# Optimization experiments

Measured on AMD Instinct MI355X. Metric: run time of the kernel, lower is better.

Reference implementation:

```python
import jax, jax.numpy as jnp
import numpy as np

B, C_IN, C_QKV, N = 8, 12, 36, 4096

def setup_inputs() -> dict:
    key = jax.random.key(0)
    ks = jax.random.split(key, 9)
    s_in = 1.0 / np.sqrt(C_IN)
    s_o = 1.0 / np.sqrt(C_QKV)
    return {
        "x": jax.random.normal(ks[0], (B, C_IN, N), dtype=jnp.float32),
        "wq": jax.random.uniform(ks[1], (C_QKV, C_IN), jnp.float32, -s_in, s_in),
        "bq": jax.random.uniform(ks[2], (C_QKV,), jnp.float32, -s_in, s_in),
        "wk": jax.random.uniform(ks[3], (C_QKV, C_IN), jnp.float32, -s_in, s_in),
        "bk": jax.random.uniform(ks[4], (C_QKV,), jnp.float32, -s_in, s_in),
        "wv": jax.random.uniform(ks[5], (C_QKV, C_IN), jnp.float32, -s_in, s_in),
        "bv": jax.random.uniform(ks[6], (C_QKV,), jnp.float32, -s_in, s_in),
        "wo": jax.random.uniform(ks[7], (C_IN, C_QKV), jnp.float32, -s_o, s_o),
        "bo": jax.random.uniform(ks[8], (C_IN,), jnp.float32, -s_o, s_o),
    }

def _conv1x1(w, b, x):
    # 1x1 Conv1d == channel-mixing matmul: [o,i] @ [b,i,n] -> [b,o,n]
    return jnp.einsum('oi,bin->bon', w, x) + b[None, :, None]

def reference(x, wq, bq, wk, bk, wv, bv, wo, bo):
    scale = 1.0 / jnp.sqrt(jnp.float32(x.shape[1]))  # 1/sqrt(12)
    q = _conv1x1(wq, bq, x)  # [B, 36, N]
    k = _conv1x1(wk, bk, x)
    v = _conv1x1(wv, bv, x)
    # inter = k^T @ q : scores[b,n,m] = sum_c k[b,c,n] * q[b,c,m]
    scores = jnp.einsum('bcn,bcm->bnm', k, q) * scale  # [B, N, N]
    weights = jax.nn.softmax(scores, axis=-1)
    attn = jnp.einsum('bcn,bnm->bcm', v, weights)  # v @ weights, [B, 36, N]
    return _conv1x1(wo, bo, attn)  # [B, 12, N]
```

## Files before the change

kernel.cpp:

```cpp
#include <hip/hip_runtime.h>
#include <hip/hip_bf16.h>
#include <math.h>

#define B 8
#define CIN 12
#define CQ 36
#define CP 48
#define N 4096
#define SCALE 0.28867513459481287f
#define LOG2E 1.4426950408889634f
#define ZSPLIT 8
#define NCHUNK (N / ZSPLIT)
#define NT (NCHUNK / 32)
#define MSPLIT 2

typedef __attribute__((ext_vector_type(4)))  short bf4_t;
typedef __attribute__((ext_vector_type(8)))  short bf8_t;
typedef __attribute__((ext_vector_type(16))) float f32x16;
typedef __attribute__((ext_vector_type(4)))  float f32x4;

__device__ __forceinline__ unsigned short f2bf(float x) {
  unsigned int u = __float_as_uint(x);
  u += 0x7FFFu + ((u >> 16) & 1u);
  return (unsigned short)(u >> 16);
}

#if __has_builtin(__builtin_amdgcn_cvt_pk_bf16_f32)
typedef __attribute__((ext_vector_type(2))) __bf16 bf16x2_t;
__device__ __forceinline__ unsigned pk2bf(float a, float b) {
  bf16x2_t v = __builtin_amdgcn_cvt_pk_bf16_f32(a, b);
  return __builtin_bit_cast(unsigned, v);
}
#else
__device__ __forceinline__ unsigned pk2bf(float a, float b) {
  return (__float_as_uint(a) >> 16) | (__float_as_uint(b) & 0xFFFF0000u);
}
#endif

__device__ __forceinline__ float bf2f(unsigned short u) {
  return __uint_as_float((unsigned)u << 16);
}

__device__ __forceinline__ float exp2fast(float x) {
#if __has_builtin(__builtin_amdgcn_exp2f)
  return __builtin_amdgcn_exp2f(x);
#else
  return exp2f(x);
#endif
}

__device__ __forceinline__ f32x4 mfma16(bf4_t a, bf4_t b, f32x4 c) {
#if __has_builtin(__builtin_amdgcn_mfma_f32_16x16x16bf16_1k)
  return __builtin_amdgcn_mfma_f32_16x16x16bf16_1k(a, b, c, 0, 0, 0);
#else
  bf8_t a8 = {a[0], a[1], a[2], a[3], 0, 0, 0, 0};
  bf8_t b8 = {b[0], b[1], b[2], b[3], 0, 0, 0, 0};
  return __builtin_amdgcn_mfma_f32_16x16x32_bf16(a8, b8, c, 0, 0, 0);
#endif
}

__device__ __forceinline__ bf8_t lds_bf8(const unsigned short* p) {
  uint2 a = *(const uint2*)p;
  uint2 b = *(const uint2*)(p + 4);
  uint4 r{a.x, a.y, b.x, b.y};
  return __builtin_bit_cast(bf8_t, r);
}
__device__ __forceinline__ void wlds16(unsigned short* p, uint4 v) {
  *(uint2*)p = uint2{v.x, v.y};
  *(uint2*)(p + 4) = uint2{v.z, v.w};
}

__global__ __launch_bounds__(256) void qkv_kernel(
    const float* __restrict__ x,
    const float* __restrict__ wq, const float* __restrict__ bq,
    const float* __restrict__ wk, const float* __restrict__ bk,
    const float* __restrict__ wv, const float* __restrict__ bv,
    unsigned short* __restrict__ qT, unsigned short* __restrict__ kT,
    unsigned short* __restrict__ vbf) {
  __shared__ float sw[CQ * CIN];
  __shared__ float sb[CQ];
  int z = blockIdx.y;
  const float* w  = (z == 0) ? wq : (z == 1) ? wk : wv;
  const float* bb = (z == 0) ? bq : (z == 1) ? bk : bv;
  float scale = (z == 1) ? SCALE * LOG2E : 1.0f;
  int tid = threadIdx.x;
  for (int e = tid; e < CQ * CIN; e += 256) sw[e] = w[e] * scale;
  if (tid < CQ) sb[tid] = bb[tid] * scale;
  __syncthreads();
  int gid = blockIdx.x * 256 + tid;
  int b = gid >> 12;
  int n = gid & (N - 1);
  float xv[CIN];
#pragma unroll
  for (int i = 0; i < CIN; ++i) xv[i] = x[(b * CIN + i) * N + n];
  if (z == 2) {
#pragma unroll
    for (int o = 0; o < CQ; ++o) {
      float a = sb[o];
#pragma unroll
      for (int i = 0; i < CIN; ++i) a += sw[o * CIN + i] * xv[i];
      vbf[((size_t)b * CP + o) * N + n] = f2bf(a);
    }
  } else {
    __attribute__((aligned(16))) unsigned row[CP / 2];
#pragma unroll
    for (int o = 0; o < CQ; o += 2) {
      float a0 = sb[o], a1 = sb[o + 1];
#pragma unroll
      for (int i = 0; i < CIN; ++i) {
        float xi = xv[i];
        a0 += sw[o * CIN + i] * xi;
        a1 += sw[(o + 1) * CIN + i] * xi;
      }
      row[o / 2] = (unsigned)f2bf(a0) | ((unsigned)f2bf(a1) << 16);
    }
    row[18] = (z == 0) ? 0x3F803F80u : 0u;
#pragma unroll
    for (int o = 19; o < CP / 2; ++o) row[o] = 0;
    unsigned short* dst = ((z == 0) ? qT : kT) + ((size_t)b * N + n) * CP;
#pragma unroll
    for (int i = 0; i < 6; ++i) *(uint4*)(dst + 8 * i) = *(const uint4*)&row[4 * i];
  }
}

__global__ __launch_bounds__(256) void stats_kernel(
    const unsigned short* __restrict__ qT, const unsigned short* __restrict__ kT,
    float* __restrict__ psum) {
  __shared__ float red[4][64];
  int tid = threadIdx.x, lane = tid & 63, wave = tid >> 6;
  int b = blockIdx.y, nblk = blockIdx.x, ms = blockIdx.z;
  int l31 = lane & 31, h = lane >> 5;
  int n0 = nblk * 64;
  size_t bN = (size_t)b * N;
  const unsigned short* krow0 = kT + (bN + n0 + l31) * CP + h * 8;
  const unsigned short* krow1 = krow0 + (size_t)32 * CP;
  bf8_t a0 = *(const bf8_t*)(krow0);
  bf8_t a1 = *(const bf8_t*)(krow0 + 16);
  bf8_t a2 = *(const bf8_t*)(krow0 + 32);
  bf8_t a3 = *(const bf8_t*)(krow1);
  bf8_t a4 = *(const bf8_t*)(krow1 + 16);
  bf8_t a5 = *(const bf8_t*)(krow1 + 32);
  float rs0[16], rs1[16];
#pragma unroll
  for (int r = 0; r < 16; ++r) { rs0[r] = 0.f; rs1[r] = 0.f; }
  const int MW = N / MSPLIT / 4;
  const unsigned short* qbase =
      qT + (bN + ms * (N / MSPLIT) + wave * MW + l31) * CP + h * 8;
#pragma unroll 2
  for (int t = 0; t < MW / 32; ++t) {
    const unsigned short* qrow2 = qbase + (size_t)t * 32 * CP;
    bf8_t b0 = *(const bf8_t*)(qrow2);
    bf8_t b1 = *(const bf8_t*)(qrow2 + 16);
    bf8_t b2 = *(const bf8_t*)(qrow2 + 32);
    f32x16 S0, S1;
#pragma unroll
    for (int r = 0; r < 16; ++r) { S0[r] = 0.f; S1[r] = 0.f; }
    S0 = __builtin_amdgcn_mfma_f32_32x32x16_bf16(a0, b0, S0, 0, 0, 0);
    S0 = __builtin_amdgcn_mfma_f32_32x32x16_bf16(a1, b1, S0, 0, 0, 0);
    S0 = __builtin_amdgcn_mfma_f32_32x32x16_bf16(a2, b2, S0, 0, 0, 0);
    S1 = __builtin_amdgcn_mfma_f32_32x32x16_bf16(a3, b0, S1, 0, 0, 0);
    S1 = __builtin_amdgcn_mfma_f32_32x32x16_bf16(a4, b1, S1, 0, 0, 0);
    S1 = __builtin_amdgcn_mfma_f32_32x32x16_bf16(a5, b2, S1, 0, 0, 0);
#pragma unroll
    for (int r = 0; r < 16; ++r) {
      rs0[r] += exp2fast(S0[r]);
      rs1[r] += exp2fast(S1[r]);
    }
  }
#pragma unroll
  for (int off = 16; off >= 1; off >>= 1)
#pragma unroll
    for (int r = 0; r < 16; ++r) {
      rs0[r] += __shfl_xor(rs0[r], off, 32);
      rs1[r] += __shfl_xor(rs1[r], off, 32);
    }
  if (l31 == 0) {
#pragma unroll
    for (int r = 0; r < 16; ++r) {
      int row = (r & 3) + 8 * (r >> 2) + 4 * h;
      red[wave][row] = rs0[r];
      red[wave][32 + row] = rs1[r];
    }
  }
  __syncthreads();
  if (tid < 64) {
    float s = red[0][tid] + red[1][tid] + red[2][tid] + red[3][tid];
    psum[((size_t)ms * B + b) * N + n0 + tid] = s;
  }
}

__global__ __launch_bounds__(256) void prep_kernel(
    const float* __restrict__ psum, unsigned short* __restrict__ kT,
    float* __restrict__ out, const float* __restrict__ bo) {
  int bx = blockIdx.x, tid = threadIdx.x;
  if (bx < B * N / 256) {
    int gid = bx * 256 + tid;
    float L = 0.f;
#pragma unroll
    for (int ms = 0; ms < MSPLIT; ++ms) L += psum[(size_t)ms * B * N + gid];
    float t = -__log2f(L);
    unsigned short hi = f2bf(t);
    unsigned short lo = f2bf(t - bf2f(hi));
    size_t base = (size_t)gid * CP;
    kT[base + 36] = hi;
    kT[base + 37] = lo;
  } else {
    int gid = (bx - B * N / 256) * 256 + tid;
    int e4 = gid * 4;
    int i = (e4 >> 12) % CIN;
    float bv = bo[i];
    *(float4*)(out + e4) = float4{bv, bv, bv, bv};
  }
}

__global__ __launch_bounds__(256, 3) void attn_kernel(
    const unsigned short* __restrict__ qT, const unsigned short* __restrict__ kT,
    const unsigned short* __restrict__ vbf, const float* __restrict__ wo,
    float* __restrict__ out) {
  __shared__ unsigned short kbuf[2][32 * 52];
  __shared__ unsigned short vbuf[2][48 * 36];
  __shared__ unsigned short plds[4][2][32 * 40];
  int tid = threadIdx.x, lane = tid & 63, wave = tid >> 6;
  int b = blockIdx.y, z = blockIdx.z, mblk = blockIdx.x;
  int l31 = lane & 31, h = lane >> 5, l15 = lane & 15, q4 = lane >> 4;
  int m0 = mblk * 256 + wave * 64;
  size_t bN = (size_t)b * N;
  bool isK0 = tid < 192;
  int r0row = isK0 ? (tid / 6) : ((tid - 192) >> 2);
  int r0c   = isK0 ? (tid % 6) : ((tid - 192) & 3);
  const unsigned short* s0 = isK0
      ? kT + (bN + z * NCHUNK + r0row) * CP + r0c * 8
      : vbf + ((size_t)b * CP + r0row) * N + z * NCHUNK + r0c * 8;
  int s0stride = isK0 ? 32 * CP : 32;
  unsigned short* dst0 = isK0 ? &kbuf[0][r0row * 52 + r0c * 8]
                              : &vbuf[0][r0row * 36 + r0c * 8];
  int dbs0 = isK0 ? 32 * 52 : 48 * 36;
  bool has1 = tid < 128;
  int r1row = (tid >> 2) + 16;
  int r1c = tid & 3;
  const unsigned short* s1 =
      vbf + ((size_t)b * CP + r1row) * N + z * NCHUNK + r1c * 8;
  unsigned short* dst1 = &vbuf[0][r1row * 36 + r1c * 8];
  const int dbs1 = 48 * 36;
  bf8_t qb[2][3];
#pragma unroll
  for (int mt = 0; mt < 2; ++mt) {
    const unsigned short* qrow = qT + (bN + m0 + mt * 32 + l31) * CP + h * 8;
    qb[mt][0] = *(const bf8_t*)(qrow);
    qb[mt][1] = *(const bf8_t*)(qrow + 16);
    qb[mt][2] = *(const bf8_t*)(qrow + 32);
  }
  bf4_t woa[3];
#pragma unroll
  for (int ct = 0; ct < 3; ++ct) {
    float4 w4 = {0.f, 0.f, 0.f, 0.f};
    int col = 16 * ct + q4 * 4;
    if (l15 < CIN && col < CQ) w4 = *(const float4*)(wo + l15 * CQ + col);
    woa[ct] = bf4_t{(short)f2bf(w4.x), (short)f2bf(w4.y),
                    (short)f2bf(w4.z), (short)f2bf(w4.w)};
  }
  f32x4 acc[2][3][2];
#pragma unroll
  for (int mt = 0; mt < 2; ++mt)
#pragma unroll
    for (int ct = 0; ct < 3; ++ct)
#pragma unroll
      for (int hm = 0; hm < 2; ++hm)
#pragma unroll
        for (int r = 0; r < 4; ++r) acc[mt][ct][hm][r] = 0.f;
  uint4 r0 = *(const uint4*)s0; s0 += s0stride;
  uint4 r1{0, 0, 0, 0};
  if (has1) { r1 = *(const uint4*)s1; s1 += 32; }
  wlds16(dst0, r0);
  if (has1) wlds16(dst1, r1);
  __syncthreads();
  for (int t = 0; t < NT; ++t) {
    int buf = t & 1;
    if (t + 1 < NT) {
      r0 = *(const uint4*)s0; s0 += s0stride;
      if (has1) { r1 = *(const uint4*)s1; s1 += 32; }
    }
    const unsigned short* kb = kbuf[buf];
    const unsigned short* vb = vbuf[buf];
    bf8_t a0 = lds_bf8(kb + l31 * 52 + h * 8);
    bf8_t a1 = lds_bf8(kb + l31 * 52 + h * 8 + 16);
    bf8_t a2 = lds_bf8(kb + l31 * 52 + h * 8 + 32);
#pragma unroll
    for (int mt = 0; mt < 2; ++mt) {
      f32x16 S;
#pragma unroll
      for (int r = 0; r < 16; ++r) S[r] = 0.f;
      S = __builtin_amdgcn_mfma_f32_32x32x16_bf16(a0, qb[mt][0], S, 0, 0, 0);
      S = __builtin_amdgcn_mfma_f32_32x32x16_bf16(a1, qb[mt][1], S, 0, 0, 0);
      S = __builtin_amdgcn_mfma_f32_32x32x16_bf16(a2, qb[mt][2], S, 0, 0, 0);
      unsigned short* pl = plds[wave][mt];
#pragma unroll
      for (int qd = 0; qd < 4; ++qd) {
        uint2 pk;
        pk.x = pk2bf(exp2fast(S[4 * qd + 0]), exp2fast(S[4 * qd + 1]));
        pk.y = pk2bf(exp2fast(S[4 * qd + 2]), exp2fast(S[4 * qd + 3]));
        *(uint2*)&pl[l31 * 40 + 8 * qd + 4 * h] = pk;
      }
    }
    bf8_t v0 = lds_bf8(vb + (0 * 16 + l15) * 36 + q4 * 8);
    bf8_t v1 = lds_bf8(vb + (1 * 16 + l15) * 36 + q4 * 8);
    bf8_t v2 = lds_bf8(vb + (2 * 16 + l15) * 36 + q4 * 8);
#pragma unroll
    for (int mt = 0; mt < 2; ++mt) {
      const unsigned short* pl = plds[wave][mt];
      bf8_t pb0 = *(const bf8_t*)&pl[l15 * 40 + q4 * 8];
      bf8_t pb1 = *(const bf8_t*)&pl[(16 + l15) * 40 + q4 * 8];
      acc[mt][0][0] = __builtin_amdgcn_mfma_f32_16x16x32_bf16(v0, pb0, acc[mt][0][0], 0, 0, 0);
      acc[mt][0][1] = __builtin_amdgcn_mfma_f32_16x16x32_bf16(v0, pb1, acc[mt][0][1], 0, 0, 0);
      acc[mt][1][0] = __builtin_amdgcn_mfma_f32_16x16x32_bf16(v1, pb0, acc[mt][1][0], 0, 0, 0);
      acc[mt][1][1] = __builtin_amdgcn_mfma_f32_16x16x32_bf16(v1, pb1, acc[mt][1][1], 0, 0, 0);
      acc[mt][2][0] = __builtin_amdgcn_mfma_f32_16x16x32_bf16(v2, pb0, acc[mt][2][0], 0, 0, 0);
      acc[mt][2][1] = __builtin_amdgcn_mfma_f32_16x16x32_bf16(v2, pb1, acc[mt][2][1], 0, 0, 0);
    }
    if (t + 1 < NT) {
      int nb = buf ^ 1;
      wlds16(dst0 + nb * dbs0, r0);
      if (has1) wlds16(dst1 + nb * dbs1, r1);
    }
    __syncthreads();
  }
#pragma unroll
  for (int mt = 0; mt < 2; ++mt)
#pragma unroll
    for (int hm = 0; hm < 2; ++hm) {
      f32x4 po = {0.f, 0.f, 0.f, 0.f};
#pragma unroll
      for (int ct = 0; ct < 3; ++ct) {
        union { uint2 u; bf4_t v; } pb;
        pb.u.x = pk2bf(acc[mt][ct][hm][0], acc[mt][ct][hm][1]);
        pb.u.y = pk2bf(acc[mt][ct][hm][2], acc[mt][ct][hm][3]);
        po = mfma16(woa[ct], pb.v, po);
      }
      if (q4 < 3) {
        float* ob = out + ((size_t)b * CIN + q4 * 4) * N + m0 + mt * 32 + hm * 16 + l15;
#pragma unroll
        for (int r = 0; r < 4; ++r) atomicAdd(ob + (size_t)r * N, po[r]);
      }
    }
}

extern "C" void kernel_launch(void* const* d_in, const int* in_sizes, int n_in,
                              void* d_out, int out_size, void* d_ws, size_t ws_size,
                              hipStream_t stream) {
  const float* x  = (const float*)d_in[0];
  const float* wq = (const float*)d_in[1];
  const float* bq = (const float*)d_in[2];
  const float* wk = (const float*)d_in[3];
  const float* bk = (const float*)d_in[4];
  const float* wv = (const float*)d_in[5];
  const float* bv = (const float*)d_in[6];
  const float* wo = (const float*)d_in[7];
  const float* bo = (const float*)d_in[8];
  float* out = (float*)d_out;

  char* ws = (char*)d_ws;
  unsigned short* qT  = (unsigned short*)ws;
  unsigned short* kT  = (unsigned short*)(ws + 3145728);
  unsigned short* vbf = (unsigned short*)(ws + 2 * 3145728);
  float* psum = (float*)(ws + 3 * 3145728);

  qkv_kernel<<<dim3(B * N / 256, 3), 256, 0, stream>>>(x, wq, bq, wk, bk, wv, bv,
                                                       qT, kT, vbf);
  stats_kernel<<<dim3(N / 64, B, MSPLIT), 256, 0, stream>>>(qT, kT, psum);
  prep_kernel<<<B * N / 256 + B * CIN * N / 1024, 256, 0, stream>>>(psum, kT, out, bo);
  attn_kernel<<<dim3(N / 256, B, ZSPLIT), 256, 0, stream>>>(qT, kT, vbf, wo, out);
}
```

Measured before the change: 137.7 us.

## Fuse four attention kernels into one persistent cooperative kernel with grid syncs

Adds a cooperative persistent kernel that runs the QKV projection, output bias init, softmax row-sum statistics and attention+output projection as phases separated by grid-wide syncs, replacing four separate launches. The log-sum computation formerly in a prep kernel is folded into the attention tile loader. This targets launch overhead and inter-kernel gaps, at the cost of grid barrier latency, a capped grid size that forces blocks to loop over work units, and LDS reuse through a union. The original multi-kernel path remains as a fallback when cooperative launch is unsupported.

```diff
diff --git a/kernel.cpp b/kernel.cpp
--- a/kernel.cpp
+++ b/kernel.cpp
@@ -1,6 +1,9 @@
 #include <hip/hip_runtime.h>
 #include <hip/hip_bf16.h>
+#include <hip/hip_cooperative_groups.h>
 #include <math.h>
+
+namespace cg = cooperative_groups;
 
 #define B 8
 #define CIN 12
@@ -68,6 +71,294 @@
 __device__ __forceinline__ void wlds16(unsigned short* p, uint4 v) {
   *(uint2*)p = uint2{v.x, v.y};
   *(uint2*)(p + 4) = uint2{v.z, v.w};
+}
+
+struct SmemAttn {
+  unsigned short kbuf[2][32 * 52];
+  unsigned short vbuf[2][48 * 36];
+  unsigned short plds[4][2][32 * 40];
+};
+union Smem {
+  SmemAttn at;
+  struct { float sw[CQ * CIN]; float sb[CQ]; } qk;
+  float red[4][64];
+};
+
+__global__ __launch_bounds__(256, 2) void fused_kernel(
+    const float* __restrict__ x,
+    const float* __restrict__ wq, const float* __restrict__ bq,
+    const float* __restrict__ wk, const float* __restrict__ bk,
+    const float* __restrict__ wv, const float* __restrict__ bv,
+    const float* __restrict__ wo, const float* __restrict__ bo,
+    unsigned short* __restrict__ qT, unsigned short* __restrict__ kT,
+    unsigned short* __restrict__ vbf, float* __restrict__ psum,
+    float* __restrict__ out) {
+  __shared__ Smem sm;
+  int tid = threadIdx.x;
+  int G = gridDim.x;
+  int lane = tid & 63, wave = tid >> 6;
+  int l31 = lane & 31, h = lane >> 5, l15 = lane & 15, q4 = lane >> 4;
+
+  for (int u = blockIdx.x; u < 384 + 384; u += G) {
+    if (u < 384) {
+      int z = u >> 7;
+      int nblk = u & 127;
+      const float* w  = (z == 0) ? wq : (z == 1) ? wk : wv;
+      const float* bb = (z == 0) ? bq : (z == 1) ? bk : bv;
+      float scale = (z == 1) ? SCALE * LOG2E : 1.0f;
+      __syncthreads();
+      for (int e = tid; e < CQ * CIN; e += 256) sm.qk.sw[e] = w[e] * scale;
+      if (tid < CQ) sm.qk.sb[tid] = bb[tid] * scale;
+      __syncthreads();
+      int gid = nblk * 256 + tid;
+      int b = gid >> 12;
+      int n = gid & (N - 1);
+      float xv[CIN];
+#pragma unroll
+      for (int i = 0; i < CIN; ++i) xv[i] = x[(b * CIN + i) * N + n];
+      if (z == 2) {
+#pragma unroll
+        for (int o = 0; o < CQ; ++o) {
+          float a = sm.qk.sb[o];
+#pragma unroll
+          for (int i = 0; i < CIN; ++i) a += sm.qk.sw[o * CIN + i] * xv[i];
+          vbf[((size_t)b * CP + o) * N + n] = f2bf(a);
+        }
+      } else {
+        __attribute__((aligned(16))) unsigned row[CP / 2];
+#pragma unroll
+        for (int o = 0; o < CQ; o += 2) {
+          float a0 = sm.qk.sb[o], a1 = sm.qk.sb[o + 1];
+#pragma unroll
+          for (int i = 0; i < CIN; ++i) {
+            float xi = xv[i];
+            a0 += sm.qk.sw[o * CIN + i] * xi;
+            a1 += sm.qk.sw[(o + 1) * CIN + i] * xi;
+          }
+          row[o / 2] = (unsigned)f2bf(a0) | ((unsigned)f2bf(a1) << 16);
+        }
+        row[18] = (z == 0) ? 0x3F803F80u : 0u;
+#pragma unroll
+        for (int o = 19; o < CP / 2; ++o) row[o] = 0;
+        unsigned short* dst = ((z == 0) ? qT : kT) + ((size_t)b * N + n) * CP;
+#pragma unroll
+        for (int i = 0; i < 6; ++i) *(uint4*)(dst + 8 * i) = *(const uint4*)&row[4 * i];
+      }
+    } else {
+      int gid4 = (u - 384) * 256 + tid;
+      int e4 = gid4 * 4;
+      int i = (e4 >> 12) % CIN;
+      float bvv = bo[i];
+      *(float4*)(out + e4) = float4{bvv, bvv, bvv, bvv};
+    }
+  }
+  __threadfence();
+  cg::this_grid().sync();
+
+  for (int u = blockIdx.x; u < 64 * B * MSPLIT; u += G) {
+    int nblk = u & 63, b = (u >> 6) & 7, ms = u >> 9;
+    __syncthreads();
+    int n0 = nblk * 64;
+    size_t bN = (size_t)b * N;
+    const unsigned short* krow0 = kT + (bN + n0 + l31) * CP + h * 8;
+    const unsigned short* krow1 = krow0 + (size_t)32 * CP;
+    bf8_t a0 = *(const bf8_t*)(krow0);
+    bf8_t a1 = *(const bf8_t*)(krow0 + 16);
+    bf8_t a2 = *(const bf8_t*)(krow0 + 32);
+    bf8_t a3 = *(const bf8_t*)(krow1);
+    bf8_t a4 = *(const bf8_t*)(krow1 + 16);
+    bf8_t a5 = *(const bf8_t*)(krow1 + 32);
+    float rs0[16], rs1[16];
+#pragma unroll
+    for (int r = 0; r < 16; ++r) { rs0[r] = 0.f; rs1[r] = 0.f; }
+    const int MW = N / MSPLIT / 4;
+    const unsigned short* qbase =
+        qT + (bN + ms * (N / MSPLIT) + wave * MW + l31) * CP + h * 8;
+#pragma unroll 2
+    for (int t = 0; t < MW / 32; ++t) {
+      const unsigned short* qrow2 = qbase + (size_t)t * 32 * CP;
+      bf8_t b0 = *(const bf8_t*)(qrow2);
+      bf8_t b1 = *(const bf8_t*)(qrow2 + 16);
+      bf8_t b2 = *(const bf8_t*)(qrow2 + 32);
+      f32x16 S0, S1;
+#pragma unroll
+      for (int r = 0; r < 16; ++r) { S0[r] = 0.f; S1[r] = 0.f; }
+      S0 = __builtin_amdgcn_mfma_f32_32x32x16_bf16(a0, b0, S0, 0, 0, 0);
+      S0 = __builtin_amdgcn_mfma_f32_32x32x16_bf16(a1, b1, S0, 0, 0, 0);
+      S0 = __builtin_amdgcn_mfma_f32_32x32x16_bf16(a2, b2, S0, 0, 0, 0);
+      S1 = __builtin_amdgcn_mfma_f32_32x32x16_bf16(a3, b0, S1, 0, 0, 0);
+      S1 = __builtin_amdgcn_mfma_f32_32x32x16_bf16(a4, b1, S1, 0, 0, 0);
+      S1 = __builtin_amdgcn_mfma_f32_32x32x16_bf16(a5, b2, S1, 0, 0, 0);
+#pragma unroll
+      for (int r = 0; r < 16; ++r) {
+        rs0[r] += exp2fast(S0[r]);
+        rs1[r] += exp2fast(S1[r]);
+      }
+    }
+#pragma unroll
+    for (int off = 16; off >= 1; off >>= 1)
+#pragma unroll
+      for (int r = 0; r < 16; ++r) {
+        rs0[r] += __shfl_xor(rs0[r], off, 32);
+        rs1[r] += __shfl_xor(rs1[r], off, 32);
+      }
+    if (l31 == 0) {
+#pragma unroll
+      for (int r = 0; r < 16; ++r) {
+        int row = (r & 3) + 8 * (r >> 2) + 4 * h;
+        sm.red[wave][row] = rs0[r];
+        sm.red[wave][32 + row] = rs1[r];
+      }
+    }
+    __syncthreads();
+    if (tid < 64) {
+      float s = sm.red[0][tid] + sm.red[1][tid] + sm.red[2][tid] + sm.red[3][tid];
+      psum[((size_t)ms * B + b) * N + n0 + tid] = s;
+    }
+  }
+  __threadfence();
+  cg::this_grid().sync();
+
+  bf4_t woa[3];
+#pragma unroll
+  for (int ct = 0; ct < 3; ++ct) {
+    float4 w4 = {0.f, 0.f, 0.f, 0.f};
+    int col = 16 * ct + q4 * 4;
+    if (l15 < CIN && col < CQ) w4 = *(const float4*)(wo + l15 * CQ + col);
+    woa[ct] = bf4_t{(short)f2bf(w4.x), (short)f2bf(w4.y),
+                    (short)f2bf(w4.z), (short)f2bf(w4.w)};
+  }
+  for (int u = blockIdx.x; u < 16 * B * ZSPLIT; u += G) {
+    int mblk = u & 15, b = (u >> 4) & 7, z = u >> 7;
+    __syncthreads();
+    int m0 = mblk * 256 + wave * 64;
+    size_t bN = (size_t)b * N;
+    bool isK0 = tid < 192;
+    int r0row = isK0 ? (tid / 6) : ((tid - 192) >> 2);
+    int r0c   = isK0 ? (tid % 6) : ((tid - 192) & 3);
+    const unsigned short* s0 = isK0
+        ? kT + (bN + z * NCHUNK + r0row) * CP + r0c * 8
+        : vbf + ((size_t)b * CP + r0row) * N + z * NCHUNK + r0c * 8;
+    int s0stride = isK0 ? 32 * CP : 32;
+    unsigned short* dst0 = isK0 ? &sm.at.kbuf[0][r0row * 52 + r0c * 8]
+                                : &sm.at.vbuf[0][r0row * 36 + r0c * 8];
+    int dbs0 = isK0 ? 32 * 52 : 48 * 36;
+    bool has1 = tid < 128;
+    int r1row = (tid >> 2) + 16;
+    int r1c = tid & 3;
+    const unsigned short* s1 =
+        vbf + ((size_t)b * CP + r1row) * N + z * NCHUNK + r1c * 8;
+    unsigned short* dst1 = &sm.at.vbuf[0][r1row * 36 + r1c * 8];
+    const int dbs1 = 48 * 36;
+    bool isP = isK0 && (r0c == 4);
+    const float* pL = psum + bN + z * NCHUNK + r0row;
+    bf8_t qb[2][3];
+#pragma unroll
+    for (int mt = 0; mt < 2; ++mt) {
+      const unsigned short* qrow = qT + (bN + m0 + mt * 32 + l31) * CP + h * 8;
+      qb[mt][0] = *(const bf8_t*)(qrow);
+      qb[mt][1] = *(const bf8_t*)(qrow + 16);
+      qb[mt][2] = *(const bf8_t*)(qrow + 32);
+    }
+    f32x4 acc[2][3][2];
+#pragma unroll
+    for (int mt = 0; mt < 2; ++mt)
+#pragma unroll
+      for (int ct = 0; ct < 3; ++ct)
+#pragma unroll
+        for (int hm = 0; hm < 2; ++hm)
+#pragma unroll
+          for (int r = 0; r < 4; ++r) acc[mt][ct][hm][r] = 0.f;
+    uint4 r0 = *(const uint4*)s0; s0 += s0stride;
+    uint4 r1{0, 0, 0, 0};
+    if (has1) { r1 = *(const uint4*)s1; s1 += 32; }
+    float Lp = 0.f;
+    if (isP) { Lp = pL[0] + pL[(size_t)B * N]; pL += 32; }
+    if (isP) {
+      float tl = -__log2f(Lp);
+      unsigned short hi = f2bf(tl);
+      unsigned short lo = f2bf(tl - bf2f(hi));
+      r0.z = (unsigned)hi | ((unsigned)lo << 16);
+    }
+    wlds16(dst0, r0);
+    if (has1) wlds16(dst1, r1);
+    __syncthreads();
+    for (int t = 0; t < NT; ++t) {
+      int buf = t & 1;
+      if (t + 1 < NT) {
+        r0 = *(const uint4*)s0; s0 += s0stride;
+        if (has1) { r1 = *(const uint4*)s1; s1 += 32; }
+        if (isP) { Lp = pL[0] + pL[(size_t)B * N]; pL += 32; }
+      }
+      const unsigned short* kb = sm.at.kbuf[buf];
+      const unsigned short* vb = sm.at.vbuf[buf];
+      bf8_t a0 = lds_bf8(kb + l31 * 52 + h * 8);
+      bf8_t a1 = lds_bf8(kb + l31 * 52 + h * 8 + 16);
+      bf8_t a2 = lds_bf8(kb + l31 * 52 + h * 8 + 32);
+#pragma unroll
+      for (int mt = 0; mt < 2; ++mt) {
+        f32x16 S;
+#pragma unroll
+        for (int r = 0; r < 16; ++r) S[r] = 0.f;
+        S = __builtin_amdgcn_mfma_f32_32x32x16_bf16(a0, qb[mt][0], S, 0, 0, 0);
+        S = __builtin_amdgcn_mfma_f32_32x32x16_bf16(a1, qb[mt][1], S, 0, 0, 0);
+        S = __builtin_amdgcn_mfma_f32_32x32x16_bf16(a2, qb[mt][2], S, 0, 0, 0);
+        unsigned short* pl = sm.at.plds[wave][mt];
+#pragma unroll
+        for (int qd = 0; qd < 4; ++qd) {
+          uint2 pk;
+          pk.x = pk2bf(exp2fast(S[4 * qd + 0]), exp2fast(S[4 * qd + 1]));
+          pk.y = pk2bf(exp2fast(S[4 * qd + 2]), exp2fast(S[4 * qd + 3]));
+          *(uint2*)&pl[l31 * 40 + 8 * qd + 4 * h] = pk;
+        }
+      }
+      bf8_t v0 = lds_bf8(vb + (0 * 16 + l15) * 36 + q4 * 8);
+      bf8_t v1 = lds_bf8(vb + (1 * 16 + l15) * 36 + q4 * 8);
+      bf8_t v2 = lds_bf8(vb + (2 * 16 + l15) * 36 + q4 * 8);
+#pragma unroll
+      for (int mt = 0; mt < 2; ++mt) {
+        const unsigned short* pl = sm.at.plds[wave][mt];
+        bf8_t pb0 = *(const bf8_t*)&pl[l15 * 40 + q4 * 8];
+        bf8_t pb1 = *(const bf8_t*)&pl[(16 + l15) * 40 + q4 * 8];
+        acc[mt][0][0] = __builtin_amdgcn_mfma_f32_16x16x32_bf16(v0, pb0, acc[mt][0][0], 0, 0, 0);
+        acc[mt][0][1] = __builtin_amdgcn_mfma_f32_16x16x32_bf16(v0, pb1, acc[mt][0][1], 0, 0, 0);
+        acc[mt][1][0] = __builtin_amdgcn_mfma_f32_16x16x32_bf16(v1, pb0, acc[mt][1][0], 0, 0, 0);
+        acc[mt][1][1] = __builtin_amdgcn_mfma_f32_16x16x32_bf16(v1, pb1, acc[mt][1][1], 0, 0, 0);
+        acc[mt][2][0] = __builtin_amdgcn_mfma_f32_16x16x32_bf16(v2, pb0, acc[mt][2][0], 0, 0, 0);
+        acc[mt][2][1] = __builtin_amdgcn_mfma_f32_16x16x32_bf16(v2, pb1, acc[mt][2][1], 0, 0, 0);
+      }
+      if (t + 1 < NT) {
+        int nb = buf ^ 1;
+        if (isP) {
+          float tl = -__log2f(Lp);
+          unsigned short hi = f2bf(tl);
+          unsigned short lo = f2bf(tl - bf2f(hi));
+          r0.z = (unsigned)hi | ((unsigned)lo << 16);
+        }
+        wlds16(dst0 + nb * dbs0, r0);
+        if (has1) wlds16(dst1 + nb * dbs1, r1);
+      }
+      __syncthreads();
+    }
+#pragma unroll
+    for (int mt = 0; mt < 2; ++mt)
+#pragma unroll
+      for (int hm = 0; hm < 2; ++hm) {
+        f32x4 po = {0.f, 0.f, 0.f, 0.f};
+#pragma unroll
+        for (int ct = 0; ct < 3; ++ct) {
+          union { uint2 u; bf4_t v; } pb;
+          pb.u.x = pk2bf(acc[mt][ct][hm][0], acc[mt][ct][hm][1]);
+          pb.u.y = pk2bf(acc[mt][ct][hm][2], acc[mt][ct][hm][3]);
+          po = mfma16(woa[ct], pb.v, po);
+        }
+        if (q4 < 3) {
+          float* ob = out + ((size_t)b * CIN + q4 * 4) * N + m0 + mt * 32 + hm * 16 + l15;
+#pragma unroll
+          for (int r = 0; r < 4; ++r) atomicAdd(ob + (size_t)r * N, po[r]);
+        }
+      }
+  }
 }
 
 __global__ __launch_bounds__(256) void qkv_kernel(
@@ -364,9 +655,33 @@
   unsigned short* vbf = (unsigned short*)(ws + 2 * 3145728);
   float* psum = (float*)(ws + 3 * 3145728);
 
-  qkv_kernel<<<dim3(B * N / 256, 3), 256, 0, stream>>>(x, wq, bq, wk, bk, wv, bv,
-                                                       qT, kT, vbf);
-  stats_kernel<<<dim3(N / 64, B, MSPLIT), 256, 0, stream>>>(qT, kT, psum);
-  prep_kernel<<<B * N / 256 + B * CIN * N / 1024, 256, 0, stream>>>(psum, kT, out, bo);
-  attn_kernel<<<dim3(N / 256, B, ZSPLIT), 256, 0, stream>>>(qT, kT, vbf, wo, out);
-}
+  static int coop = -1;
+  static int grid_blocks = 0;
+  if (coop < 0) {
+    int c = 0;
+    if (hipDeviceGetAttribute(&c, hipDeviceAttributeCooperativeLaunch, 0) != hipSuccess)
+      c = 0;
+    int nb = 0, ncu = 0;
+    hipOccupancyMaxActiveBlocksPerMultiprocessor(&nb, fused_kernel, 256, 0);
+    hipDeviceGetAttribute(&ncu, hipDeviceAttributeMultiprocessorCount, 0);
+    if (nb < 1) nb = 1;
+    if (ncu < 1) ncu = 256;
+    long cap = (long)nb * ncu;
+    grid_blocks = (int)(cap < 512 ? cap : 512);
+    coop = (c && grid_blocks >= 1) ? 1 : 0;
+  }
+
+  if (coop) {
+    void* args[] = { (void*)&x, (void*)&wq, (void*)&bq, (void*)&wk, (void*)&bk,
+                     (void*)&wv, (void*)&bv, (void*)&wo, (void*)&bo,
+                     (void*)&qT, (void*)&kT, (void*)&vbf, (void*)&psum, (void*)&out };
+    hipLaunchCooperativeKernel((const void*)fused_kernel, dim3(grid_blocks),
+                               dim3(256), args, 0, stream);
+  } else {
+    qkv_kernel<<<dim3(B * N / 256, 3), 256, 0, stream>>>(x, wq, bq, wk, bk, wv, bv,
+                                                         qT, kT, vbf);
+    stats_kernel<<<dim3(N / 64, B, MSPLIT), 256, 0, stream>>>(qT, kT, psum);
+    prep_kernel<<<B * N / 256 + B * CIN * N / 1024, 256, 0, stream>>>(psum, kT, out, bo);
+    attn_kernel<<<dim3(N / 256, B, ZSPLIT), 256, 0, stream>>>(qT, kT, vbf, wo, out);
+  }
+}
```

Result: slower. 308.2 us (+123.9%).

## Remove prep kernel by fusing bias init into qkv and log-sum into attn loads

Applied to the files above, without the earlier changes.

Drops the separate prep kernel. The output bias fill moves into an extra blockIdx.y slice of the qkv kernel. The per-key log-normaliser (-log2 of the summed partial exponentials) is now computed inside the attention kernel's K-tile loader and patched into the staged K row before the LDS write. This removes one launch and a global round trip for kT columns 36/37, but the log is recomputed by each of the 16 m-blocks that load the same K chunk, and the loader threads gain extra psum loads.

```diff
diff --git a/kernel.cpp b/kernel.cpp
--- a/kernel.cpp
+++ b/kernel.cpp
@@ -75,15 +75,27 @@
     const float* __restrict__ wq, const float* __restrict__ bq,
     const float* __restrict__ wk, const float* __restrict__ bk,
     const float* __restrict__ wv, const float* __restrict__ bv,
+    const float* __restrict__ bo,
     unsigned short* __restrict__ qT, unsigned short* __restrict__ kT,
-    unsigned short* __restrict__ vbf) {
+    unsigned short* __restrict__ vbf, float* __restrict__ out) {
   __shared__ float sw[CQ * CIN];
   __shared__ float sb[CQ];
   int z = blockIdx.y;
+  int tid = threadIdx.x;
+  if (z == 3) {
+#pragma unroll
+    for (int r = 0; r < 3; ++r) {
+      int gid4 = blockIdx.x * 256 + tid + r * 32768;
+      int e4 = gid4 * 4;
+      int i = (e4 >> 12) % CIN;
+      float bvv = bo[i];
+      *(float4*)(out + e4) = float4{bvv, bvv, bvv, bvv};
+    }
+    return;
+  }
   const float* w  = (z == 0) ? wq : (z == 1) ? wk : wv;
   const float* bb = (z == 0) ? bq : (z == 1) ? bk : bv;
   float scale = (z == 1) ? SCALE * LOG2E : 1.0f;
-  int tid = threadIdx.x;
   for (int e = tid; e < CQ * CIN; e += 256) sw[e] = w[e] * scale;
   if (tid < CQ) sb[tid] = bb[tid] * scale;
   __syncthreads();
@@ -189,34 +201,10 @@
   }
 }
 
-__global__ __launch_bounds__(256) void prep_kernel(
-    const float* __restrict__ psum, unsigned short* __restrict__ kT,
-    float* __restrict__ out, const float* __restrict__ bo) {
-  int bx = blockIdx.x, tid = threadIdx.x;
-  if (bx < B * N / 256) {
-    int gid = bx * 256 + tid;
-    float L = 0.f;
-#pragma unroll
-    for (int ms = 0; ms < MSPLIT; ++ms) L += psum[(size_t)ms * B * N + gid];
-    float t = -__log2f(L);
-    unsigned short hi = f2bf(t);
-    unsigned short lo = f2bf(t - bf2f(hi));
-    size_t base = (size_t)gid * CP;
-    kT[base + 36] = hi;
-    kT[base + 37] = lo;
-  } else {
-    int gid = (bx - B * N / 256) * 256 + tid;
-    int e4 = gid * 4;
-    int i = (e4 >> 12) % CIN;
-    float bv = bo[i];
-    *(float4*)(out + e4) = float4{bv, bv, bv, bv};
-  }
-}
-
 __global__ __launch_bounds__(256, 3) void attn_kernel(
     const unsigned short* __restrict__ qT, const unsigned short* __restrict__ kT,
     const unsigned short* __restrict__ vbf, const float* __restrict__ wo,
-    float* __restrict__ out) {
+    const float* __restrict__ psum, float* __restrict__ out) {
   __shared__ unsigned short kbuf[2][32 * 52];
   __shared__ unsigned short vbuf[2][48 * 36];
   __shared__ unsigned short plds[4][2][32 * 40];
@@ -242,6 +230,8 @@
       vbf + ((size_t)b * CP + r1row) * N + z * NCHUNK + r1c * 8;
   unsigned short* dst1 = &vbuf[0][r1row * 36 + r1c * 8];
   const int dbs1 = 48 * 36;
+  bool isP = isK0 && (r0c == 4);
+  const float* pL = psum + bN + z * NCHUNK + r0row;
   bf8_t qb[2][3];
 #pragma unroll
   for (int mt = 0; mt < 2; ++mt) {
@@ -271,6 +261,14 @@
   uint4 r0 = *(const uint4*)s0; s0 += s0stride;
   uint4 r1{0, 0, 0, 0};
   if (has1) { r1 = *(const uint4*)s1; s1 += 32; }
+  float Lp = 0.f;
+  if (isP) { Lp = pL[0] + pL[(size_t)B * N]; pL += 32; }
+  if (isP) {
+    float tl = -__log2f(Lp);
+    unsigned short hi = f2bf(tl);
+    unsigned short lo = f2bf(tl - bf2f(hi));
+    r0.z = (unsigned)hi | ((unsigned)lo << 16);
+  }
   wlds16(dst0, r0);
   if (has1) wlds16(dst1, r1);
   __syncthreads();
@@ -279,6 +277,7 @@
     if (t + 1 < NT) {
       r0 = *(const uint4*)s0; s0 += s0stride;
       if (has1) { r1 = *(const uint4*)s1; s1 += 32; }
+      if (isP) { Lp = pL[0] + pL[(size_t)B * N]; pL += 32; }
     }
     const unsigned short* kb = kbuf[buf];
     const unsigned short* vb = vbuf[buf];
@@ -319,6 +318,12 @@
     }
     if (t + 1 < NT) {
       int nb = buf ^ 1;
+      if (isP) {
+        float tl = -__log2f(Lp);
+        unsigned short hi = f2bf(tl);
+        unsigned short lo = f2bf(tl - bf2f(hi));
+        r0.z = (unsigned)hi | ((unsigned)lo << 16);
+      }
       wlds16(dst0 + nb * dbs0, r0);
       if (has1) wlds16(dst1 + nb * dbs1, r1);
     }
@@ -364,9 +369,8 @@
   unsigned short* vbf = (unsigned short*)(ws + 2 * 3145728);
   float* psum = (float*)(ws + 3 * 3145728);
 
-  qkv_kernel<<<dim3(B * N / 256, 3), 256, 0, stream>>>(x, wq, bq, wk, bk, wv, bv,
-                                                       qT, kT, vbf);
+  qkv_kernel<<<dim3(B * N / 256, 4), 256, 0, stream>>>(x, wq, bq, wk, bk, wv, bv,
+                                                       bo, qT, kT, vbf, out);
   stats_kernel<<<dim3(N / 64, B, MSPLIT), 256, 0, stream>>>(qT, kT, psum);
-  prep_kernel<<<B * N / 256 + B * CIN * N / 1024, 256, 0, stream>>>(psum, kT, out, bo);
-  attn_kernel<<<dim3(N / 256, B, ZSPLIT), 256, 0, stream>>>(qT, kT, vbf, wo, out);
-}
+  attn_kernel<<<dim3(N / 256, B, ZSPLIT), 256, 0, stream>>>(qT, kT, vbf, wo, psum, out);
+}
```

Result: slower. 143.0 us (+3.8%).
